# Performance work log

Hardware: AMD Instinct MI355X
Metric: run time of the kernel (lower is better)

Reference implementation:

```python
import jax, jax.numpy as jnp
import numpy as np
import math

R = 3  # search_radius (init_kwargs)


def _normalize(x, eps=1e-6):
    # F.normalize(x, dim=1): x / max(||x||_2, eps)
    n = jnp.sqrt(jnp.sum(x * x, axis=1, keepdims=True))
    return x / jnp.maximum(n, eps)


def setup_inputs() -> dict:
    key = jax.random.key(0)
    k1, k2 = jax.random.split(key)
    B, D, H, W = 8, 64, 256, 256
    rubin_2d = jax.random.normal(k1, (B, D, H, W), dtype=jnp.float32)
    vis_2d = jax.random.normal(k2, (B, D, H, W), dtype=jnp.float32)
    log_temperature = jnp.asarray(math.log(0.1), dtype=jnp.float32)
    return {"rubin_2d": rubin_2d, "vis_2d": vis_2d, "log_temperature": log_temperature}


def reference(rubin_2d, vis_2d, log_temperature):
    B, D, H, W = rubin_2d.shape
    r = R
    K = (2 * r + 1) ** 2
    rubin_n = _normalize(rubin_2d)
    vis_n = _normalize(vis_2d)
    # replicate padding == 'edge'
    vis_pad = jnp.pad(vis_n, ((0, 0), (0, 0), (r, r), (r, r)), mode="edge")
    scale = 1.0 / math.sqrt(float(max(1, D)))
    # K=(2r+1)^2 shifted correlation maps (small fixed loop over displacements)
    corrs = []
    for dy in range(-r, r + 1):
        for dx in range(-r, r + 1):
            shifted = vis_pad[:, :, r + dy:r + dy + H, r + dx:r + dx + W]
            corrs.append(jnp.sum(rubin_n * shifted, axis=1) * scale)  # [B,H,W]
    logits = jnp.stack(corrs, axis=1)  # [B,K,H,W]

    offs = np.arange(-r, r + 1, dtype=np.float32)
    dy_lut = jnp.asarray(np.repeat(offs, 2 * r + 1)).reshape(1, K, 1, 1)
    dx_lut = jnp.asarray(np.tile(offs, 2 * r + 1)).reshape(1, K, 1, 1)

    tau = jnp.maximum(jnp.exp(log_temperature), 1e-3)
    probs_local = jax.nn.softmax(logits / tau, axis=1)  # [B,K,H,W]
    dy_local = jnp.sum(probs_local * dy_lut, axis=1, keepdims=True)
    dx_local = jnp.sum(probs_local * dx_lut, axis=1, keepdims=True)
    conf_local = jnp.max(probs_local, axis=1, keepdims=True)

    logits_global = jnp.mean(logits, axis=(2, 3), keepdims=True)  # [B,K,1,1]
    probs_global = jax.nn.softmax(logits_global / tau, axis=1)
    dy_global = jnp.sum(probs_global * dy_lut, axis=1, keepdims=True)
    dx_global = jnp.sum(probs_global * dx_lut, axis=1, keepdims=True)
    conf_global = jnp.max(probs_global, axis=1, keepdims=True)

    uniform = 1.0 / float(max(1, K))
    local_weight = jnp.clip((conf_local - uniform) / max(1e-6, 1.0 - uniform), 0.0, 1.0)
    dy = local_weight * dy_local + (1.0 - local_weight) * dy_global
    dx = local_weight * dx_local + (1.0 - local_weight) * dx_global
    return (dy, dx, conf_local, conf_global, local_weight, logits)
```

## Files before the change

### kernel.cpp

```cpp
#include <hip/hip_runtime.h>

#define HDIM 256
#define WDIM 256
#define DDIM 64
#define HWSZ (HDIM*WDIM)
#define NPIX 524288

#define TW 32
#define TH 16
#define BT 512
#define HW_T 38
#define HH_T 22
#define NPX 836
#define DC 8
#define NCH 8
#define PSTR 12

#define OFF_DY   0
#define OFF_DX   524288
#define OFF_CONF 1048576
#define OFF_CG   1572864
#define OFF_LW   1572872
#define OFF_LG   2097160

#define WS_GACC 0
#define WS_DYG  392
#define WS_DXG  400

__global__ void zero_ws_k(float* __restrict__ ws) {
    const int i = threadIdx.x;
    if (i < 408) ws[i] = 0.f;
}

__global__ void __launch_bounds__(BT, 4)
corr_main_k(const float* __restrict__ rub, const float* __restrict__ vis,
            const float* __restrict__ ltemp, float* __restrict__ out,
            float* __restrict__ ws)
{
    __shared__ __align__(16) float vis_s[NPX * PSTR];
    __shared__ float invv_s[NPX];
    __shared__ float gacc_s[49];

    const int tid = threadIdx.x;
    const int tx  = tid & 31;
    const int ty  = tid >> 5;
    const int w0  = blockIdx.x * TW;
    const int h0  = blockIdx.y * TH;
    const int b   = blockIdx.z;
    const int ibase = b * (DDIM * HWSZ);

    if (tid < 49) gacc_s[tid] = 0.f;

    const bool val1 = (tid + BT) < NPX;
    const int px1c  = val1 ? (tid + BT) : (NPX - 1);
    auto halo_goff = [&](int px) -> int {
        const int hr = px / HW_T;
        const int wc = px - hr * HW_T;
        const int gh = min(HDIM - 1, max(0, h0 - 3 + hr));
        const int gw = min(WDIM - 1, max(0, w0 - 3 + wc));
        return gh * WDIM + gw;
    };
    const int goff0 = halo_goff(tid);
    const int goff1 = halo_goff(px1c);
    const int pown  = (h0 + ty) * WDIM + (w0 + tx);
    const int l0 = tid * PSTR;
    const int l1 = px1c * PSTR;

    float acc[49];
#pragma unroll
    for (int k = 0; k < 49; ++k) acc[k] = 0.f;
    float sq0 = 0.f, sq1 = 0.f, sr = 0.f;

    float vv0[DC], vv1[DC], rcur[DC], rnext[DC];
#pragma unroll
    for (int d = 0; d < DC; ++d) {
        const int gof = ibase + d * HWSZ;
        vv0[d]  = vis[gof + goff0];
        vv1[d]  = vis[gof + goff1];
        rcur[d] = rub[gof + pown];
    }

    const float* vb = &vis_s[(ty * HW_T + tx) * PSTR];

#pragma unroll 1
    for (int c = 0; c < NCH; ++c) {
        __syncthreads();
        *reinterpret_cast<float4*>(&vis_s[l0])     = make_float4(vv0[0], vv0[1], vv0[2], vv0[3]);
        *reinterpret_cast<float4*>(&vis_s[l0 + 4]) = make_float4(vv0[4], vv0[5], vv0[6], vv0[7]);
        *reinterpret_cast<float4*>(&vis_s[l1])     = make_float4(vv1[0], vv1[1], vv1[2], vv1[3]);
        *reinterpret_cast<float4*>(&vis_s[l1 + 4]) = make_float4(vv1[4], vv1[5], vv1[6], vv1[7]);
#pragma unroll
        for (int d = 0; d < DC; ++d) { sq0 += vv0[d] * vv0[d]; sq1 += vv1[d] * vv1[d]; }
        __syncthreads();

        if (c < NCH - 1) {
#pragma unroll
            for (int d = 0; d < DC; ++d) {
                const int gof = ibase + ((c + 1) * DC + d) * HWSZ;
                vv0[d]  = vis[gof + goff0];
                vv1[d]  = vis[gof + goff1];
                rnext[d] = rub[gof + pown];
            }
        }

#pragma unroll
        for (int g = 0; g < 2; ++g) {
            const float a0 = rcur[4*g+0], a1 = rcur[4*g+1], a2 = rcur[4*g+2], a3 = rcur[4*g+3];
#pragma unroll
            for (int dyi = 0; dyi < 7; ++dyi) {
#pragma unroll
                for (int dxi = 0; dxi < 7; ++dxi) {
                    const float4 v = *reinterpret_cast<const float4*>(
                        vb + (dyi * HW_T + dxi) * PSTR + 4 * g);
                    float a = acc[dyi * 7 + dxi];
                    a = fmaf(a0, v.x, a); a = fmaf(a1, v.y, a);
                    a = fmaf(a2, v.z, a); a = fmaf(a3, v.w, a);
                    acc[dyi * 7 + dxi] = a;
                }
            }
        }
#pragma unroll
        for (int d = 0; d < DC; ++d) sr += rcur[d] * rcur[d];
#pragma unroll
        for (int d = 0; d < DC; ++d) rcur[d] = rnext[d];
    }

    invv_s[tid] = 1.f / fmaxf(sqrtf(sq0), 1e-6f);
    if (val1) invv_s[tid + BT] = 1.f / fmaxf(sqrtf(sq1), 1e-6f);
    __syncthreads();

    const float tau  = fmaxf(__expf(ltemp[0]), 1e-3f);
    const float itau = 1.f / tau;
    const float invr = 1.f / fmaxf(sqrtf(sr), 1e-6f);
    const float cR   = invr * 0.125f;
    const float uu   = 1.f / 49.f;
    const float i1mu = 49.f / 48.f;

    const int h = h0 + ty, w = w0 + tx;
    const int lgbase = OFF_LG + b * 49 * HWSZ + h * WDIM + w;
    float mlg = -1e30f;
#pragma unroll
    for (int dyi = 0; dyi < 7; ++dyi) {
        const int rowb = (ty + dyi) * HW_T + tx;
#pragma unroll
        for (int dxi = 0; dxi < 7; ++dxi) {
            const int k = dyi * 7 + dxi;
            const float lg = acc[k] * cR * invv_s[rowb + dxi];
            out[lgbase + k * HWSZ] = lg;
            acc[k] = lg;
            mlg = fmaxf(mlg, lg);
        }
    }
    const float m = mlg * itau;
    float S = 0.f, sdy = 0.f, sdx = 0.f;
#pragma unroll
    for (int dyi = 0; dyi < 7; ++dyi) {
#pragma unroll
        for (int dxi = 0; dxi < 7; ++dxi) {
            const float e = __expf(fmaf(acc[dyi * 7 + dxi], itau, -m));
            S += e;
            sdy += e * (float)(dyi - 3);
            sdx += e * (float)(dxi - 3);
        }
    }
    const float invS = 1.f / S;
    const float conf = invS;
    const float lw   = fminf(fmaxf((conf - uu) * i1mu, 0.f), 1.f);
    const int po = b * HWSZ + h * WDIM + w;
    out[OFF_CONF + po] = conf;
    out[OFF_LW   + po] = lw;
    out[OFF_DY   + po] = sdy * invS;
    out[OFF_DX   + po] = sdx * invS;

#pragma unroll
    for (int k = 0; k < 49; ++k) {
        float v = acc[k];
#pragma unroll
        for (int off = 32; off > 0; off >>= 1)
            v += __shfl_xor(v, off, 64);
        if ((tid & 63) == 0) atomicAdd(&gacc_s[k], v);
    }
    __syncthreads();
    if (tid < 49) atomicAdd(&ws[WS_GACC + b * 49 + tid], gacc_s[tid]);
}

__global__ void glob_branch_k(const float* __restrict__ ltemp,
                              float* __restrict__ out, float* __restrict__ ws)
{
    const int t = threadIdx.x;
    if (t >= 8) return;
    const float tau  = fmaxf(__expf(ltemp[0]), 1e-3f);
    const float itau = 1.f / tau;
    float tk[49];
    float m = -1e30f;
#pragma unroll
    for (int k = 0; k < 49; ++k) {
        const float mean = ws[WS_GACC + t * 49 + k] * (1.f / 65536.f);
        tk[k] = mean * itau;
        m = fmaxf(m, tk[k]);
    }
    float S = 0.f, sdy = 0.f, sdx = 0.f;
#pragma unroll
    for (int k = 0; k < 49; ++k) {
        const float e = __expf(tk[k] - m);
        S += e;
        sdy += e * (float)(k / 7 - 3);
        sdx += e * (float)(k % 7 - 3);
    }
    const float invS = 1.f / S;
    out[OFF_CG + t] = invS;
    ws[WS_DYG + t] = sdy * invS;
    ws[WS_DXG + t] = sdx * invS;
}

__global__ void combine_k(float* __restrict__ out, const float* __restrict__ ws)
{
    const int gid = blockIdx.x * 256 + threadIdx.x;
    if (gid >= NPIX) return;
    const int b = gid >> 16;
    const float lw  = out[OFF_LW + gid];
    const float dyl = out[OFF_DY + gid];
    const float dxl = out[OFF_DX + gid];
    out[OFF_DY + gid] = lw * dyl + (1.f - lw) * ws[WS_DYG + b];
    out[OFF_DX + gid] = lw * dxl + (1.f - lw) * ws[WS_DXG + b];
}

extern "C" void kernel_launch(void* const* d_in, const int* in_sizes, int n_in,
                              void* d_out, int out_size, void* d_ws, size_t ws_size,
                              hipStream_t stream)
{
    const float* rub = (const float*)d_in[0];
    const float* vis = (const float*)d_in[1];
    const float* lt  = (const float*)d_in[2];
    float* out = (float*)d_out;
    float* ws  = (float*)d_ws;

    hipLaunchKernelGGL(zero_ws_k, dim3(1), dim3(512), 0, stream, ws);
    hipLaunchKernelGGL(corr_main_k, dim3(WDIM / TW, HDIM / TH, 8), dim3(BT), 0, stream,
                       rub, vis, lt, out, ws);
    hipLaunchKernelGGL(glob_branch_k, dim3(1), dim3(64), 0, stream, lt, out, ws);
    hipLaunchKernelGGL(combine_k, dim3(NPIX / 256), dim3(256), 0, stream, out, ws);
}
```

Before: 396.5 us.

## Store vis tile in fp16 and accumulate correlations with packed fdot2

Inputs are converted to fp16 pairs on load, so the shared-memory tile holds 16 channels per pixel in two 16-byte slots instead of 8 fp32 values. The correlation inner loop uses v_dot2 fp16 instructions with fp32 accumulation, and the norms are computed the same way. Four chunks replace eight, which halves the number of barriers and per-channel LDS reads. The occupancy hint drops to 2 blocks per CU. Rounding inputs to fp16 loses precision in the logits, and with a temperature of 0.1 the softmax may amplify that error.

```diff
diff --git a/kernel.cpp b/kernel.cpp
--- a/kernel.cpp
+++ b/kernel.cpp
@@ -1,4 +1,6 @@
 #include <hip/hip_runtime.h>
+
+typedef _Float16 half2_t __attribute__((ext_vector_type(2)));
 
 #define HDIM 256
 #define WDIM 256
@@ -12,9 +14,8 @@
 #define HW_T 38
 #define HH_T 22
 #define NPX 836
-#define DC 8
-#define NCH 8
-#define PSTR 12
+#define DC 16
+#define NCH 4
 
 #define OFF_DY   0
 #define OFF_DX   524288
@@ -27,17 +28,19 @@
 #define WS_DYG  392
 #define WS_DXG  400
 
+struct alignas(16) H8 { half2_t v[4]; };
+
 __global__ void zero_ws_k(float* __restrict__ ws) {
     const int i = threadIdx.x;
     if (i < 408) ws[i] = 0.f;
 }
 
-__global__ void __launch_bounds__(BT, 4)
+__global__ void __launch_bounds__(BT, 2)
 corr_main_k(const float* __restrict__ rub, const float* __restrict__ vis,
             const float* __restrict__ ltemp, float* __restrict__ out,
             float* __restrict__ ws)
 {
-    __shared__ __align__(16) float vis_s[NPX * PSTR];
+    __shared__ H8 vis_s[NPX * 2];
     __shared__ float invv_s[NPX];
     __shared__ float gacc_s[49];
 
@@ -63,66 +66,75 @@
     const int goff0 = halo_goff(tid);
     const int goff1 = halo_goff(px1c);
     const int pown  = (h0 + ty) * WDIM + (w0 + tx);
-    const int l0 = tid * PSTR;
-    const int l1 = px1c * PSTR;
 
     float acc[49];
 #pragma unroll
     for (int k = 0; k < 49; ++k) acc[k] = 0.f;
     float sq0 = 0.f, sq1 = 0.f, sr = 0.f;
 
-    float vv0[DC], vv1[DC], rcur[DC], rnext[DC];
-#pragma unroll
-    for (int d = 0; d < DC; ++d) {
-        const int gof = ibase + d * HWSZ;
-        vv0[d]  = vis[gof + goff0];
-        vv1[d]  = vis[gof + goff1];
-        rcur[d] = rub[gof + pown];
-    }
-
-    const float* vb = &vis_s[(ty * HW_T + tx) * PSTR];
+    half2_t vv0[8], vv1[8], rcur[8], rnext[8];
+
+    auto load_chunk = [&](int c, half2_t* v0, half2_t* v1, half2_t* rr) {
+#pragma unroll
+        for (int j = 0; j < 8; ++j) {
+            const int gof0 = ibase + (c * DC + 2 * j) * HWSZ;
+            const int gof1 = gof0 + HWSZ;
+            half2_t a; a[0] = (_Float16)vis[gof0 + goff0]; a[1] = (_Float16)vis[gof1 + goff0];
+            half2_t bb; bb[0] = (_Float16)vis[gof0 + goff1]; bb[1] = (_Float16)vis[gof1 + goff1];
+            half2_t r; r[0] = (_Float16)rub[gof0 + pown];  r[1] = (_Float16)rub[gof1 + pown];
+            v0[j] = a; v1[j] = bb; rr[j] = r;
+        }
+    };
+    load_chunk(0, vv0, vv1, rcur);
+
+    const int rowbase = ty * HW_T + tx;
 
 #pragma unroll 1
     for (int c = 0; c < NCH; ++c) {
         __syncthreads();
-        *reinterpret_cast<float4*>(&vis_s[l0])     = make_float4(vv0[0], vv0[1], vv0[2], vv0[3]);
-        *reinterpret_cast<float4*>(&vis_s[l0 + 4]) = make_float4(vv0[4], vv0[5], vv0[6], vv0[7]);
-        *reinterpret_cast<float4*>(&vis_s[l1])     = make_float4(vv1[0], vv1[1], vv1[2], vv1[3]);
-        *reinterpret_cast<float4*>(&vis_s[l1 + 4]) = make_float4(vv1[4], vv1[5], vv1[6], vv1[7]);
-#pragma unroll
-        for (int d = 0; d < DC; ++d) { sq0 += vv0[d] * vv0[d]; sq1 += vv1[d] * vv1[d]; }
+        {
+            H8 w;
+            w.v[0] = vv0[0]; w.v[1] = vv0[1]; w.v[2] = vv0[2]; w.v[3] = vv0[3];
+            vis_s[tid] = w;
+            w.v[0] = vv0[4]; w.v[1] = vv0[5]; w.v[2] = vv0[6]; w.v[3] = vv0[7];
+            vis_s[NPX + tid] = w;
+            w.v[0] = vv1[0]; w.v[1] = vv1[1]; w.v[2] = vv1[2]; w.v[3] = vv1[3];
+            vis_s[px1c] = w;
+            w.v[0] = vv1[4]; w.v[1] = vv1[5]; w.v[2] = vv1[6]; w.v[3] = vv1[7];
+            vis_s[NPX + px1c] = w;
+        }
+#pragma unroll
+        for (int j = 0; j < 8; ++j) {
+            sq0 = __builtin_amdgcn_fdot2(vv0[j], vv0[j], sq0, false);
+            sq1 = __builtin_amdgcn_fdot2(vv1[j], vv1[j], sq1, false);
+            sr  = __builtin_amdgcn_fdot2(rcur[j], rcur[j], sr, false);
+        }
         __syncthreads();
 
-        if (c < NCH - 1) {
-#pragma unroll
-            for (int d = 0; d < DC; ++d) {
-                const int gof = ibase + ((c + 1) * DC + d) * HWSZ;
-                vv0[d]  = vis[gof + goff0];
-                vv1[d]  = vis[gof + goff1];
-                rnext[d] = rub[gof + pown];
+        if (c < NCH - 1)
+            load_chunk(c + 1, vv0, vv1, rnext);
+
+#pragma unroll
+        for (int dyi = 0; dyi < 7; ++dyi) {
+            const int rp = rowbase + dyi * HW_T;
+#pragma unroll
+            for (int dxi = 0; dxi < 7; ++dxi) {
+                const H8 p = vis_s[rp + dxi];
+                const H8 q = vis_s[NPX + rp + dxi];
+                float a = acc[dyi * 7 + dxi];
+                a = __builtin_amdgcn_fdot2(rcur[0], p.v[0], a, false);
+                a = __builtin_amdgcn_fdot2(rcur[1], p.v[1], a, false);
+                a = __builtin_amdgcn_fdot2(rcur[2], p.v[2], a, false);
+                a = __builtin_amdgcn_fdot2(rcur[3], p.v[3], a, false);
+                a = __builtin_amdgcn_fdot2(rcur[4], q.v[0], a, false);
+                a = __builtin_amdgcn_fdot2(rcur[5], q.v[1], a, false);
+                a = __builtin_amdgcn_fdot2(rcur[6], q.v[2], a, false);
+                a = __builtin_amdgcn_fdot2(rcur[7], q.v[3], a, false);
+                acc[dyi * 7 + dxi] = a;
             }
         }
-
-#pragma unroll
-        for (int g = 0; g < 2; ++g) {
-            const float a0 = rcur[4*g+0], a1 = rcur[4*g+1], a2 = rcur[4*g+2], a3 = rcur[4*g+3];
-#pragma unroll
-            for (int dyi = 0; dyi < 7; ++dyi) {
-#pragma unroll
-                for (int dxi = 0; dxi < 7; ++dxi) {
-                    const float4 v = *reinterpret_cast<const float4*>(
-                        vb + (dyi * HW_T + dxi) * PSTR + 4 * g);
-                    float a = acc[dyi * 7 + dxi];
-                    a = fmaf(a0, v.x, a); a = fmaf(a1, v.y, a);
-                    a = fmaf(a2, v.z, a); a = fmaf(a3, v.w, a);
-                    acc[dyi * 7 + dxi] = a;
-                }
-            }
-        }
-#pragma unroll
-        for (int d = 0; d < DC; ++d) sr += rcur[d] * rcur[d];
-#pragma unroll
-        for (int d = 0; d < DC; ++d) rcur[d] = rnext[d];
+#pragma unroll
+        for (int j = 0; j < 8; ++j) rcur[j] = rnext[j];
     }
 
     invv_s[tid] = 1.f / fmaxf(sqrtf(sq0), 1e-6f);
```

New measurement: 409.9 us. 1.03x slower.
